# Performance work log

Hardware: AMD Instinct MI355X
Metric: run time of the kernel (lower is better)

Reference implementation:

```python
import jax, jax.numpy as jnp
import numpy as np

OBS = 128; N_AGENT = 16; N_ACTION = 8; N_LAYER = 2; HID = 128
GE = 256; LE = 256; F1 = 512; F2 = 512


def _edges(batch_size, n):
    # all ordered pairs (i, j), i != j, within each sample; GCNConv adds self-loops
    i, j = np.meshgrid(np.arange(n), np.arange(n), indexing='ij')
    m = i != j
    src0, dst0 = i[m], j[m]                      # [n*(n-1)]
    off = (np.arange(batch_size) * n)[:, None]
    src = (src0[None, :] + off).reshape(-1)
    dst = (dst0[None, :] + off).reshape(-1)
    return jnp.asarray(src, jnp.int32), jnp.asarray(dst, jnp.int32)


def setup_inputs() -> dict:
    key = jax.random.key(0)
    ks = jax.random.split(key, 16)
    g = lambda k, shp, fan: jax.random.normal(k, shp, jnp.float32) / np.sqrt(fan)
    return {
        'obs_j': jax.random.normal(ks[0], (2048, N_AGENT, OBS), jnp.float32),
        'W_pre': g(ks[1], (OBS, HID), OBS), 'b_pre': jnp.zeros((HID,), jnp.float32),
        'W_gcn': g(ks[2], (N_LAYER, HID, HID), HID), 'b_gcn': jnp.zeros((N_LAYER, HID), jnp.float32),
        'W_post': g(ks[3], (HID, GE), HID), 'b_post': jnp.zeros((GE,), jnp.float32),
        'W_loc': g(ks[4], (OBS, LE), OBS), 'b_loc': jnp.zeros((LE,), jnp.float32),
        'W1': g(ks[5], (GE + LE, F1), GE + LE), 'b1': jnp.zeros((F1,), jnp.float32),
        'W2': g(ks[6], (F1, F2), F1), 'b2': jnp.zeros((F2,), jnp.float32),
        'W3': g(ks[7], (F2, N_ACTION), F2), 'b3': jnp.zeros((N_ACTION,), jnp.float32),
    }


def reference(obs_j, W_pre, b_pre, W_gcn, b_gcn, W_post, b_post,
              W_loc, b_loc, W1, b1, W2, b2, W3, b3):
    B, n, _ = obs_j.shape
    N = B * n
    obs = obs_j.reshape(N, OBS)
    x = jax.nn.relu(obs @ W_pre + b_pre)          # [N, HID]

    src, dst = _edges(B, n)
    # GCNConv with self-loops on a fully-connected graph: deg = n for every node,
    # edge norm = 1/sqrt(deg_i*deg_j) = 1/n for every (A+I) edge.
    inv_n = jnp.float32(1.0) / n
    for l in range(N_LAYER):
        h = x @ W_gcn[l]                          # lin (no bias inside propagate)
        agg = jax.ops.segment_sum(h[src], dst, num_segments=N)  # neighbor gather/scatter
        x = jax.nn.relu((agg + h) * inv_n + b_gcn[l])            # + self-loop msg, bias

    g = x.reshape(B, n, HID).mean(axis=1)         # global_mean_pool over each graph
    g = jax.nn.relu(g @ W_post + b_post)          # [B, GE]
    loc = jax.nn.relu(obs @ W_loc + b_loc)        # [B*n, LE]
    gi = jnp.repeat(g, n, axis=0)                 # repeat_interleave over agents
    z = jnp.concatenate([gi, loc], axis=1)
    z = jax.nn.relu(z @ W1 + b1)
    z = jax.nn.relu(z @ W2 + b2)
    q = z @ W3 + b3
    return q.reshape(B, n, N_ACTION)
```

## Files before the change

kernel.cpp:

```cpp
#include <hip/hip_runtime.h>
#include <hip/hip_bf16.h>
#include <stdint.h>

typedef __bf16 bf16;
typedef __bf16 bf16x4 __attribute__((ext_vector_type(4)));
typedef __bf16 bf16x8 __attribute__((ext_vector_type(8)));
typedef float f32x4 __attribute__((ext_vector_type(4)));

#define BM 128
#define BN 128
#define BK 64

#define GL(p) ((const __attribute__((address_space(1))) void*)(p))
#define SH(p) ((__attribute__((address_space(3))) void*)(p))

__device__ inline void tp(const float* W, bf16* WT, int id, int shiftK, int N) {
  int K = 1 << shiftK;
  int n = id >> shiftK;
  int k = id & (K - 1);
  WT[id] = (bf16)W[(size_t)k * N + n];
}

__global__ __launch_bounds__(256) void prep_all(
    const float* __restrict__ W1, const float* __restrict__ W2,
    bf16* __restrict__ W1T, bf16* __restrict__ W2T,
    const float* __restrict__ Wpre, const float* __restrict__ Wloc,
    const float* __restrict__ Wgcn, const float* __restrict__ Wpost,
    bf16* __restrict__ WpreLocT, bf16* __restrict__ Wg0T, bf16* __restrict__ Wg1T,
    bf16* __restrict__ WpostT,
    const float* __restrict__ bpre, const float* __restrict__ bloc,
    float* __restrict__ biasPL, float* __restrict__ outq) {
  __shared__ bf16 tile[64 * 68];
  int blk = blockIdx.x;
  int tid = threadIdx.x;
  if (blk < 128) {
    const float* W = (blk < 64) ? W1 : W2;
    bf16* WT = (blk < 64) ? W1T : W2T;
    int t = blk & 63;
    int tk0 = (t >> 3) * 64, tn0 = (t & 7) * 64;
#pragma unroll
    for (int p = 0; p < 4; p++) {
      int kr = p * 16 + (tid >> 4), nc = (tid & 15) * 4;
      float4 f = *(const float4*)(W + (size_t)(tk0 + kr) * 512 + tn0 + nc);
      bf16x4 v; v[0] = (bf16)f.x; v[1] = (bf16)f.y; v[2] = (bf16)f.z; v[3] = (bf16)f.w;
      *(bf16x4*)&tile[kr * 68 + nc] = v;
    }
    __syncthreads();
#pragma unroll
    for (int p = 0; p < 4; p++) {
      int nr = p * 16 + (tid >> 4), kc = (tid & 15) * 4;
      bf16x4 v;
#pragma unroll
      for (int i = 0; i < 4; i++) v[i] = tile[(kc + i) * 68 + nr];
      *(bf16x4*)(WT + (size_t)(tn0 + nr) * 512 + tk0 + kc) = v;
    }
    return;
  }
  blk -= 128;
  if (blk < 448) {
    int id = blk * 256 + tid;
    if (id < 16384) { tp(Wpre, WpreLocT, id, 7, 128); return; } id -= 16384;
    if (id < 32768) { tp(Wloc, WpreLocT + 16384, id, 7, 256); return; } id -= 32768;
    if (id < 16384) { tp(Wgcn, Wg0T, id, 7, 128); return; } id -= 16384;
    if (id < 16384) { tp(Wgcn + 16384, Wg1T, id, 7, 128); return; } id -= 16384;
    tp(Wpost, WpostT, id, 7, 256);
    return;
  }
  blk -= 448;
  if (blk == 0) {
    if (tid < 128) biasPL[tid] = bpre[tid];
    biasPL[128 + tid] = bloc[tid];
    return;
  }
  blk -= 1;
  float4 z = {0.f, 0.f, 0.f, 0.f};
#pragma unroll
  for (int i = 0; i < 4; i++)
    ((float4*)outq)[(size_t)blk * 1024 + i * 256 + tid] = z;
}

template <int NT, int ASRC, bool POOL, bool QFUSE>
__global__ __launch_bounds__(256, 4) void gemm_k(
    const float* __restrict__ Af, const bf16* __restrict__ Ab, const bf16* __restrict__ Ag,
    const bf16* __restrict__ BT, const float* __restrict__ bias,
    bf16* __restrict__ C, int ldc, bf16* __restrict__ pool_out,
    const float* __restrict__ W3, const float* __restrict__ b3, float* __restrict__ outq,
    int M, int K) {
  __shared__ bf16 smem[16384];
  bf16* As = smem;
  bf16* Bs = smem + 8192;

  const int tid = threadIdx.x;
  const int id = blockIdx.x;
  const int s = id >> 3;
  const int n_idx = s % NT;
  const int m0 = ((id & 7) + 8 * (s / NT)) * BM;
  const int n0 = n_idx * BN;

  f32x4 acc[4][4] = {};

  const int lane = tid & 63;
  const int wave = tid >> 6;
  const int wm = (wave >> 1) * 64;
  const int wn = (wave & 1) * 64;
  const int lm = lane & 15;
  const int quad = lane >> 4;

  for (int k0 = 0; k0 < K; k0 += BK) {
#pragma unroll
    for (int it = 0; it < 4; it++) {
      int idx = it * 256 + tid;
      int row = idx >> 3;
      int c = idx & 7;
      int cv8 = c ^ (row & 7);
      int kk = k0 + cv8 * 8;
      if (ASRC == 1) {
        const float* src = Af + (size_t)(m0 + row) * K + kk;
        float4 f0 = *(const float4*)src;
        float4 f1 = *(const float4*)(src + 4);
        bf16x8 v;
        v[0] = (bf16)f0.x; v[1] = (bf16)f0.y; v[2] = (bf16)f0.z; v[3] = (bf16)f0.w;
        v[4] = (bf16)f1.x; v[5] = (bf16)f1.y; v[6] = (bf16)f1.z; v[7] = (bf16)f1.w;
        *(bf16x8*)&As[row * 64 + c * 8] = v;
      } else {
        const bf16* ga;
        if (ASRC == 2) {
          int r = m0 + row;
          ga = (k0 < 256) ? (Ag + (size_t)(r >> 4) * 256 + kk)
                          : (Ab + (size_t)r * 256 + (kk - 256));
        } else {
          ga = Ab + (size_t)(m0 + row) * K + kk;
        }
        __builtin_amdgcn_global_load_lds(GL(ga), SH(&As[(idx & ~63) * 8]), 16, 0, 0);
      }
      const bf16* gb = BT + (size_t)(n0 + row) * K + kk;
      __builtin_amdgcn_global_load_lds(GL(gb), SH(&Bs[(idx & ~63) * 8]), 16, 0, 0);
    }
    __syncthreads();

#pragma unroll
    for (int ks = 0; ks < 2; ks++) {
      const int ua = quad + ks * 4;
      bf16x8 a[4], b[4];
#pragma unroll
      for (int i = 0; i < 4; i++) {
        int r = wm + lm + i * 16;
        a[i] = *(const bf16x8*)&As[r * 64 + ((ua ^ (r & 7)) * 8)];
      }
#pragma unroll
      for (int j = 0; j < 4; j++) {
        int r = wn + lm + j * 16;
        b[j] = *(const bf16x8*)&Bs[r * 64 + ((ua ^ (r & 7)) * 8)];
      }
#pragma unroll
      for (int i = 0; i < 4; i++)
#pragma unroll
        for (int j = 0; j < 4; j++)
          acc[i][j] = __builtin_amdgcn_mfma_f32_16x16x32_bf16(a[i], b[j], acc[i][j], 0, 0, 0);
    }
    __syncthreads();
  }

  if (POOL && n_idx == 0) {
#pragma unroll
    for (int i = 0; i < 4; i++) {
      int sample = (m0 + wm + i * 16) >> 4;
#pragma unroll
      for (int j = 0; j < 4; j++) {
        int col = wn + j * 16 + lm;
        float b = bias[col];
        float v = 0.f;
#pragma unroll
        for (int r = 0; r < 4; r++) v += fmaxf(acc[i][j][r] + b, 0.f);
        v += __shfl_xor(v, 16);
        v += __shfl_xor(v, 32);
        if (quad == 0) pool_out[(size_t)sample * 128 + col] = (bf16)(v * 0.0625f);
      }
    }
  } else if (QFUSE) {
#pragma unroll
    for (int i = 0; i < 4; i++)
#pragma unroll
      for (int j = 0; j < 4; j++) {
        int col = wn + j * 16 + lm;
        float b = bias[n0 + col];
#pragma unroll
        for (int r = 0; r < 4; r++) {
          int row = wm + i * 16 + quad * 4 + r;
          smem[row * 128 + col] = (bf16)fmaxf(acc[i][j][r] + b, 0.f);
        }
      }
    __syncthreads();
    int n = lane & 7;
    int kg = lane >> 3;
    float w3r[16];
#pragma unroll
    for (int i = 0; i < 16; i++) w3r[i] = W3[(size_t)(n0 + kg * 16 + i) * 8 + n];
    float bn = (n_idx == 0) ? b3[n] : 0.f;
    int rbase = wave * 32;
    for (int rr = 0; rr < 32; rr++) {
      const bf16* zr = &smem[(rbase + rr) * 128 + kg * 16];
      bf16x8 z0 = *(const bf16x8*)zr;
      bf16x8 z1v = *(const bf16x8*)(zr + 8);
      float v = 0.f;
#pragma unroll
      for (int i = 0; i < 8; i++) v += (float)z0[i] * w3r[i];
#pragma unroll
      for (int i = 0; i < 8; i++) v += (float)z1v[i] * w3r[8 + i];
      v += __shfl_down(v, 32);
      v += __shfl_down(v, 16);
      v += __shfl_down(v, 8);
      if (lane < 8) atomicAdd(&outq[(size_t)(m0 + rbase + rr) * 8 + n], v + bn);
    }
  } else {
#pragma unroll
    for (int i = 0; i < 4; i++)
#pragma unroll
      for (int j = 0; j < 4; j++) {
        int col = wn + j * 16 + lm;
        float b = bias[n0 + col];
#pragma unroll
        for (int r = 0; r < 4; r++) {
          int row = wm + i * 16 + quad * 4 + r;
          smem[row * 128 + col] = (bf16)fmaxf(acc[i][j][r] + b, 0.f);
        }
      }
    __syncthreads();
    const int coff = POOL ? (n0 - 128) : n0;
#pragma unroll
    for (int c = 0; c < 8; c++) {
      int ci = c * 256 + tid;
      int row = ci >> 4, col8 = (ci & 15) * 8;
      *(bf16x8*)&C[(size_t)(m0 + row) * ldc + coff + col8] = *(const bf16x8*)&smem[row * 128 + col8];
    }
  }
}

__global__ __launch_bounds__(256) void gcn_chain(
    const bf16* __restrict__ xbar, const bf16* __restrict__ Wg0T,
    const bf16* __restrict__ Wg1T, const bf16* __restrict__ WpostT,
    const float* __restrict__ b_gcn, const float* __restrict__ b_post,
    bf16* __restrict__ g) {
  __shared__ bf16 xs[16 * 136];
  __shared__ bf16 ws[256 * 136];
  const int tid = threadIdx.x;
  const int lane = tid & 63, wave = tid >> 6;
  const int lm = lane & 15, quad = lane >> 4;
  const int rb = blockIdx.x * 16;

  {
    int row = tid >> 4, cv = (tid & 15) * 8;
    *(bf16x8*)&xs[row * 136 + cv] = *(const bf16x8*)&xbar[(size_t)(rb + row) * 128 + cv];
  }

  const bf16* Wl[3] = {Wg0T, Wg1T, WpostT};
  const float* bl[3] = {b_gcn, b_gcn + 128, b_post};
  const int Nl[3] = {128, 128, 256};

  for (int l = 0; l < 3; l++) {
    const int N = Nl[l];
    __syncthreads();
    for (int c = tid; c < N * 16; c += 256) {
      int row = c >> 4, cv = (c & 15) * 8;
      *(bf16x8*)&ws[row * 136 + cv] = *(const bf16x8*)&Wl[l][(size_t)row * 128 + cv];
    }
    __syncthreads();
    const int nj = N / 64;
    f32x4 acc[4] = {};
#pragma unroll
    for (int kk = 0; kk < 128; kk += 32) {
      bf16x8 a = *(const bf16x8*)&xs[lm * 136 + quad * 8 + kk];
      for (int j = 0; j < nj; j++) {
        int col = (wave * nj + j) * 16 + lm;
        bf16x8 b = *(const bf16x8*)&ws[col * 136 + quad * 8 + kk];
        acc[j] = __builtin_amdgcn_mfma_f32_16x16x32_bf16(a, b, acc[j], 0, 0, 0);
      }
    }
    __syncthreads();
    const float* bias = bl[l];
    if (l < 2) {
      for (int j = 0; j < nj; j++) {
        int col = (wave * nj + j) * 16 + lm;
        float bv = bias[col];
#pragma unroll
        for (int r = 0; r < 4; r++)
          xs[(quad * 4 + r) * 136 + col] = (bf16)fmaxf(acc[j][r] + bv, 0.f);
      }
    } else {
      for (int j = 0; j < nj; j++) {
        int col = (wave * nj + j) * 16 + lm;
        float bv = bias[col];
#pragma unroll
        for (int r = 0; r < 4; r++)
          g[(size_t)(rb + quad * 4 + r) * 256 + col] = (bf16)fmaxf(acc[j][r] + bv, 0.f);
      }
    }
  }
}

extern "C" void kernel_launch(void* const* d_in, const int* in_sizes, int n_in,
                              void* d_out, int out_size, void* d_ws, size_t ws_size,
                              hipStream_t stream) {
  const float* obs    = (const float*)d_in[0];
  const float* W_pre  = (const float*)d_in[1];
  const float* b_pre  = (const float*)d_in[2];
  const float* W_gcn  = (const float*)d_in[3];
  const float* b_gcn  = (const float*)d_in[4];
  const float* W_post = (const float*)d_in[5];
  const float* b_post = (const float*)d_in[6];
  const float* W_loc  = (const float*)d_in[7];
  const float* b_loc  = (const float*)d_in[8];
  const float* W1     = (const float*)d_in[9];
  const float* b1     = (const float*)d_in[10];
  const float* W2     = (const float*)d_in[11];
  const float* b2     = (const float*)d_in[12];
  const float* W3     = (const float*)d_in[13];
  const float* b3     = (const float*)d_in[14];
  float* out = (float*)d_out;

  char* p = (char*)d_ws;
  auto alloc = [&](size_t bytes) { char* r = p; p += (bytes + 255) & ~(size_t)255; return r; };
  bf16* WpreLocT = (bf16*)alloc(384 * 128 * 2);
  float* biasPL  = (float*)alloc(384 * 4);
  bf16* Wg0T   = (bf16*)alloc(128 * 128 * 2);
  bf16* Wg1T   = (bf16*)alloc(128 * 128 * 2);
  bf16* WpostT = (bf16*)alloc(256 * 128 * 2);
  bf16* W1T    = (bf16*)alloc(512 * 512 * 2);
  bf16* W2T    = (bf16*)alloc(512 * 512 * 2);
  bf16* xbar   = (bf16*)alloc(2048 * 128 * 2);
  bf16* loc    = (bf16*)alloc((size_t)32768 * 256 * 2);
  bf16* g      = (bf16*)alloc(2048 * 256 * 2);
  bf16* z1     = (bf16*)alloc((size_t)32768 * 512 * 2);

  prep_all<<<641, 256, 0, stream>>>(W1, W2, W1T, W2T,
                                    W_pre, W_loc, W_gcn, W_post,
                                    WpreLocT, Wg0T, Wg1T, WpostT,
                                    b_pre, b_loc, biasPL, out);
  gemm_k<3, 1, true, false><<<768, 256, 0, stream>>>(
      obs, nullptr, nullptr, WpreLocT, biasPL, loc, 256, xbar,
      nullptr, nullptr, nullptr, 32768, 128);
  gcn_chain<<<128, 256, 0, stream>>>(xbar, Wg0T, Wg1T, WpostT, b_gcn, b_post, g);
  gemm_k<4, 2, false, false><<<1024, 256, 0, stream>>>(
      nullptr, loc, g, W1T, b1, z1, 512, nullptr,
      nullptr, nullptr, nullptr, 32768, 512);
  gemm_k<4, 0, false, true><<<1024, 256, 0, stream>>>(
      nullptr, z1, nullptr, W2T, b2, nullptr, 0, nullptr,
      W3, b3, out, 32768, 512);
}
```

Measured before the change: 174.3 us.

## Fuse GCN chain into first GEMM's pooling blocks, removing a kernel launch

The separate gcn_chain kernel is removed. The n_idx==0 blocks of the first GEMM now take their pooled 8-sample tile (padded to 16 rows) and run the two GCN layers and the post-projection with MFMA in the same block, writing g directly. The xbar round trip and one launch go away, and the GEMM kernels are specialised with compile-time K. In exchange, a third of the first kernel's blocks do extra serial work with weights read straight from global memory, and half of each MFMA tile is wasted on padding rows.

Result: faster. 169.3 us (-2.9%).

```diff
diff --git a/kernel.cpp b/kernel.cpp
--- a/kernel.cpp
+++ b/kernel.cpp
@@ -7,10 +7,7 @@
 typedef __bf16 bf16x8 __attribute__((ext_vector_type(8)));
 typedef float f32x4 __attribute__((ext_vector_type(4)));
 
-#define BM 128
-#define BN 128
-#define BK 64
-
+#define MFMA(a, b, c) __builtin_amdgcn_mfma_f32_16x16x32_bf16(a, b, c, 0, 0, 0)
 #define GL(p) ((const __attribute__((address_space(1))) void*)(p))
 #define SH(p) ((__attribute__((address_space(3))) void*)(p))
 
@@ -79,13 +76,13 @@
     ((float4*)outq)[(size_t)blk * 1024 + i * 256 + tid] = z;
 }
 
-template <int NT, int ASRC, bool POOL, bool QFUSE>
-__global__ __launch_bounds__(256, 4) void gemm_k(
-    const float* __restrict__ Af, const bf16* __restrict__ Ab, const bf16* __restrict__ Ag,
-    const bf16* __restrict__ BT, const float* __restrict__ bias,
-    bf16* __restrict__ C, int ldc, bf16* __restrict__ pool_out,
-    const float* __restrict__ W3, const float* __restrict__ b3, float* __restrict__ outq,
-    int M, int K) {
+__global__ __launch_bounds__(256, 4) void k1c(
+    const float* __restrict__ obs, const bf16* __restrict__ WpreLocT,
+    const float* __restrict__ biasPL,
+    const bf16* __restrict__ Wg0T, const bf16* __restrict__ Wg1T,
+    const bf16* __restrict__ WpostT, const float* __restrict__ b_gcn,
+    const float* __restrict__ b_post,
+    bf16* __restrict__ loc, bf16* __restrict__ g) {
   __shared__ bf16 smem[16384];
   bf16* As = smem;
   bf16* Bs = smem + 8192;
@@ -93,20 +90,16 @@
   const int tid = threadIdx.x;
   const int id = blockIdx.x;
   const int s = id >> 3;
-  const int n_idx = s % NT;
-  const int m0 = ((id & 7) + 8 * (s / NT)) * BM;
-  const int n0 = n_idx * BN;
+  const int n_idx = s % 3;
+  const int m0 = ((id & 7) + 8 * (s / 3)) * 128;
+  const int n0 = n_idx * 128;
 
   f32x4 acc[4][4] = {};
-
-  const int lane = tid & 63;
-  const int wave = tid >> 6;
-  const int wm = (wave >> 1) * 64;
-  const int wn = (wave & 1) * 64;
-  const int lm = lane & 15;
-  const int quad = lane >> 4;
-
-  for (int k0 = 0; k0 < K; k0 += BK) {
+  const int lane = tid & 63, wave = tid >> 6;
+  const int wm = (wave >> 1) * 64, wn = (wave & 1) * 64;
+  const int lm = lane & 15, quad = lane >> 4;
+
+  for (int k0 = 0; k0 < 128; k0 += 64) {
 #pragma unroll
     for (int it = 0; it < 4; it++) {
       int idx = it * 256 + tid;
@@ -114,30 +107,17 @@
       int c = idx & 7;
       int cv8 = c ^ (row & 7);
       int kk = k0 + cv8 * 8;
-      if (ASRC == 1) {
-        const float* src = Af + (size_t)(m0 + row) * K + kk;
-        float4 f0 = *(const float4*)src;
-        float4 f1 = *(const float4*)(src + 4);
-        bf16x8 v;
-        v[0] = (bf16)f0.x; v[1] = (bf16)f0.y; v[2] = (bf16)f0.z; v[3] = (bf16)f0.w;
-        v[4] = (bf16)f1.x; v[5] = (bf16)f1.y; v[6] = (bf16)f1.z; v[7] = (bf16)f1.w;
-        *(bf16x8*)&As[row * 64 + c * 8] = v;
-      } else {
-        const bf16* ga;
-        if (ASRC == 2) {
-          int r = m0 + row;
-          ga = (k0 < 256) ? (Ag + (size_t)(r >> 4) * 256 + kk)
-                          : (Ab + (size_t)r * 256 + (kk - 256));
-        } else {
-          ga = Ab + (size_t)(m0 + row) * K + kk;
-        }
-        __builtin_amdgcn_global_load_lds(GL(ga), SH(&As[(idx & ~63) * 8]), 16, 0, 0);
-      }
-      const bf16* gb = BT + (size_t)(n0 + row) * K + kk;
+      const float* src = obs + (size_t)(m0 + row) * 128 + kk;
+      float4 f0 = *(const float4*)src;
+      float4 f1 = *(const float4*)(src + 4);
+      bf16x8 v;
+      v[0] = (bf16)f0.x; v[1] = (bf16)f0.y; v[2] = (bf16)f0.z; v[3] = (bf16)f0.w;
+      v[4] = (bf16)f1.x; v[5] = (bf16)f1.y; v[6] = (bf16)f1.z; v[7] = (bf16)f1.w;
+      *(bf16x8*)&As[row * 64 + c * 8] = v;
+      const bf16* gb = WpreLocT + (size_t)(n0 + row) * 128 + kk;
       __builtin_amdgcn_global_load_lds(GL(gb), SH(&Bs[(idx & ~63) * 8]), 16, 0, 0);
     }
     __syncthreads();
-
 #pragma unroll
     for (int ks = 0; ks < 2; ks++) {
       const int ua = quad + ks * 4;
@@ -156,38 +136,204 @@
       for (int i = 0; i < 4; i++)
 #pragma unroll
         for (int j = 0; j < 4; j++)
-          acc[i][j] = __builtin_amdgcn_mfma_f32_16x16x32_bf16(a[i], b[j], acc[i][j], 0, 0, 0);
-    }
-    __syncthreads();
-  }
-
-  if (POOL && n_idx == 0) {
+          acc[i][j] = MFMA(a[i], b[j], acc[i][j]);
+    }
+    __syncthreads();
+  }
+
+  if (n_idx == 0) {
+    bf16* xs = smem;
+    bf16* x2 = smem + 2176;
 #pragma unroll
     for (int i = 0; i < 4; i++) {
-      int sample = (m0 + wm + i * 16) >> 4;
+      int sl = (wave >> 1) * 4 + i;
 #pragma unroll
       for (int j = 0; j < 4; j++) {
         int col = wn + j * 16 + lm;
-        float b = bias[col];
+        float bb = biasPL[col];
         float v = 0.f;
 #pragma unroll
-        for (int r = 0; r < 4; r++) v += fmaxf(acc[i][j][r] + b, 0.f);
+        for (int r = 0; r < 4; r++) v += fmaxf(acc[i][j][r] + bb, 0.f);
         v += __shfl_xor(v, 16);
         v += __shfl_xor(v, 32);
-        if (quad == 0) pool_out[(size_t)sample * 128 + col] = (bf16)(v * 0.0625f);
-      }
-    }
-  } else if (QFUSE) {
+        if (quad == 0) xs[sl * 136 + col] = (bf16)(v * 0.0625f);
+        else if (quad == 1) xs[(8 + sl) * 136 + col] = (bf16)0.f;
+      }
+    }
+    __syncthreads();
+    {
+      f32x4 c2[2] = {};
+#pragma unroll
+      for (int ku = 0; ku < 4; ++ku) {
+        bf16x8 a = *(const bf16x8*)&xs[lm * 136 + (ku * 4 + quad) * 8];
+#pragma unroll
+        for (int jn = 0; jn < 2; ++jn) {
+          int col = (wave * 2 + jn) * 16 + lm;
+          bf16x8 b = *(const bf16x8*)&Wg0T[(size_t)col * 128 + ku * 32 + quad * 8];
+          c2[jn] = MFMA(a, b, c2[jn]);
+        }
+      }
+      __syncthreads();
+#pragma unroll
+      for (int jn = 0; jn < 2; ++jn) {
+        int col = (wave * 2 + jn) * 16 + lm;
+        float bb = b_gcn[col];
+#pragma unroll
+        for (int r = 0; r < 4; ++r)
+          x2[(quad * 4 + r) * 136 + col] = (bf16)fmaxf(c2[jn][r] + bb, 0.f);
+      }
+    }
+    __syncthreads();
+    {
+      f32x4 c2[2] = {};
+#pragma unroll
+      for (int ku = 0; ku < 4; ++ku) {
+        bf16x8 a = *(const bf16x8*)&x2[lm * 136 + (ku * 4 + quad) * 8];
+#pragma unroll
+        for (int jn = 0; jn < 2; ++jn) {
+          int col = (wave * 2 + jn) * 16 + lm;
+          bf16x8 b = *(const bf16x8*)&Wg1T[(size_t)col * 128 + ku * 32 + quad * 8];
+          c2[jn] = MFMA(a, b, c2[jn]);
+        }
+      }
+      __syncthreads();
+#pragma unroll
+      for (int jn = 0; jn < 2; ++jn) {
+        int col = (wave * 2 + jn) * 16 + lm;
+        float bb = b_gcn[128 + col];
+#pragma unroll
+        for (int r = 0; r < 4; ++r)
+          xs[(quad * 4 + r) * 136 + col] = (bf16)fmaxf(c2[jn][r] + bb, 0.f);
+      }
+    }
+    __syncthreads();
+    {
+      f32x4 c3[4] = {};
+#pragma unroll
+      for (int ku = 0; ku < 4; ++ku) {
+        bf16x8 a = *(const bf16x8*)&xs[lm * 136 + (ku * 4 + quad) * 8];
+#pragma unroll
+        for (int jn = 0; jn < 4; ++jn) {
+          int col = (wave * 4 + jn) * 16 + lm;
+          bf16x8 b = *(const bf16x8*)&WpostT[(size_t)col * 128 + ku * 32 + quad * 8];
+          c3[jn] = MFMA(a, b, c3[jn]);
+        }
+      }
+      int sample0 = m0 >> 4;
+#pragma unroll
+      for (int jn = 0; jn < 4; ++jn) {
+        int col = (wave * 4 + jn) * 16 + lm;
+        float bb = b_post[col];
+#pragma unroll
+        for (int r = 0; r < 4; ++r) {
+          int row = quad * 4 + r;
+          if (row < 8)
+            g[(size_t)(sample0 + row) * 256 + col] = (bf16)fmaxf(c3[jn][r] + bb, 0.f);
+        }
+      }
+    }
+  } else {
 #pragma unroll
     for (int i = 0; i < 4; i++)
 #pragma unroll
       for (int j = 0; j < 4; j++) {
         int col = wn + j * 16 + lm;
-        float b = bias[n0 + col];
+        float bb = biasPL[n0 + col];
 #pragma unroll
         for (int r = 0; r < 4; r++) {
           int row = wm + i * 16 + quad * 4 + r;
-          smem[row * 128 + col] = (bf16)fmaxf(acc[i][j][r] + b, 0.f);
+          smem[row * 128 + col] = (bf16)fmaxf(acc[i][j][r] + bb, 0.f);
+        }
+      }
+    __syncthreads();
+    const int coff = n0 - 128;
+#pragma unroll
+    for (int c = 0; c < 8; c++) {
+      int ci = c * 256 + tid;
+      int row = ci >> 4, col8 = (ci & 15) * 8;
+      *(bf16x8*)&loc[(size_t)(m0 + row) * 256 + coff + col8] = *(const bf16x8*)&smem[row * 128 + col8];
+    }
+  }
+}
+
+template <int ASRC, bool QFUSE>
+__global__ __launch_bounds__(256, 4) void gemm_k(
+    const bf16* __restrict__ Ab, const bf16* __restrict__ Ag,
+    const bf16* __restrict__ BT, const float* __restrict__ bias,
+    bf16* __restrict__ C,
+    const float* __restrict__ W3, const float* __restrict__ b3,
+    float* __restrict__ outq) {
+  __shared__ bf16 smem[16384];
+  bf16* As = smem;
+  bf16* Bs = smem + 8192;
+
+  const int tid = threadIdx.x;
+  const int id = blockIdx.x;
+  const int s = id >> 3;
+  const int n_idx = s & 3;
+  const int m0 = ((id & 7) + 8 * (s >> 2)) * 128;
+  const int n0 = n_idx * 128;
+
+  f32x4 acc[4][4] = {};
+  const int lane = tid & 63, wave = tid >> 6;
+  const int wm = (wave >> 1) * 64, wn = (wave & 1) * 64;
+  const int lm = lane & 15, quad = lane >> 4;
+
+  for (int k0 = 0; k0 < 512; k0 += 64) {
+#pragma unroll
+    for (int it = 0; it < 4; it++) {
+      int idx = it * 256 + tid;
+      int row = idx >> 3;
+      int c = idx & 7;
+      int cv8 = c ^ (row & 7);
+      int kk = k0 + cv8 * 8;
+      const bf16* ga;
+      if (ASRC == 2) {
+        int r = m0 + row;
+        ga = (k0 < 256) ? (Ag + (size_t)(r >> 4) * 256 + kk)
+                        : (Ab + (size_t)r * 256 + (kk - 256));
+      } else {
+        ga = Ab + (size_t)(m0 + row) * 512 + kk;
+      }
+      __builtin_amdgcn_global_load_lds(GL(ga), SH(&As[(idx & ~63) * 8]), 16, 0, 0);
+      const bf16* gb = BT + (size_t)(n0 + row) * 512 + kk;
+      __builtin_amdgcn_global_load_lds(GL(gb), SH(&Bs[(idx & ~63) * 8]), 16, 0, 0);
+    }
+    __syncthreads();
+#pragma unroll
+    for (int ks = 0; ks < 2; ks++) {
+      const int ua = quad + ks * 4;
+      bf16x8 a[4], b[4];
+#pragma unroll
+      for (int i = 0; i < 4; i++) {
+        int r = wm + lm + i * 16;
+        a[i] = *(const bf16x8*)&As[r * 64 + ((ua ^ (r & 7)) * 8)];
+      }
+#pragma unroll
+      for (int j = 0; j < 4; j++) {
+        int r = wn + lm + j * 16;
+        b[j] = *(const bf16x8*)&Bs[r * 64 + ((ua ^ (r & 7)) * 8)];
+      }
+#pragma unroll
+      for (int i = 0; i < 4; i++)
+#pragma unroll
+        for (int j = 0; j < 4; j++)
+          acc[i][j] = MFMA(a[i], b[j], acc[i][j]);
+    }
+    __syncthreads();
+  }
+
+  if (QFUSE) {
+#pragma unroll
+    for (int i = 0; i < 4; i++)
+#pragma unroll
+      for (int j = 0; j < 4; j++) {
+        int col = wn + j * 16 + lm;
+        float bb = bias[n0 + col];
+#pragma unroll
+        for (int r = 0; r < 4; r++) {
+          int row = wm + i * 16 + quad * 4 + r;
+          smem[row * 128 + col] = (bf16)fmaxf(acc[i][j][r] + bb, 0.f);
         }
       }
     __syncthreads();
@@ -218,82 +364,19 @@
 #pragma unroll
       for (int j = 0; j < 4; j++) {
         int col = wn + j * 16 + lm;
-        float b = bias[n0 + col];
+        float bb = bias[n0 + col];
 #pragma unroll
         for (int r = 0; r < 4; r++) {
           int row = wm + i * 16 + quad * 4 + r;
-          smem[row * 128 + col] = (bf16)fmaxf(acc[i][j][r] + b, 0.f);
-        }
-      }
-    __syncthreads();
-    const int coff = POOL ? (n0 - 128) : n0;
+          smem[row * 128 + col] = (bf16)fmaxf(acc[i][j][r] + bb, 0.f);
+        }
+      }
+    __syncthreads();
 #pragma unroll
     for (int c = 0; c < 8; c++) {
       int ci = c * 256 + tid;
       int row = ci >> 4, col8 = (ci & 15) * 8;
-      *(bf16x8*)&C[(size_t)(m0 + row) * ldc + coff + col8] = *(const bf16x8*)&smem[row * 128 + col8];
-    }
-  }
-}
-
-__global__ __launch_bounds__(256) void gcn_chain(
-    const bf16* __restrict__ xbar, const bf16* __restrict__ Wg0T,
-    const bf16* __restrict__ Wg1T, const bf16* __restrict__ WpostT,
-    const float* __restrict__ b_gcn, const float* __restrict__ b_post,
-    bf16* __restrict__ g) {
-  __shared__ bf16 xs[16 * 136];
-  __shared__ bf16 ws[256 * 136];
-  const int tid = threadIdx.x;
-  const int lane = tid & 63, wave = tid >> 6;
-  const int lm = lane & 15, quad = lane >> 4;
-  const int rb = blockIdx.x * 16;
-
-  {
-    int row = tid >> 4, cv = (tid & 15) * 8;
-    *(bf16x8*)&xs[row * 136 + cv] = *(const bf16x8*)&xbar[(size_t)(rb + row) * 128 + cv];
-  }
-
-  const bf16* Wl[3] = {Wg0T, Wg1T, WpostT};
-  const float* bl[3] = {b_gcn, b_gcn + 128, b_post};
-  const int Nl[3] = {128, 128, 256};
-
-  for (int l = 0; l < 3; l++) {
-    const int N = Nl[l];
-    __syncthreads();
-    for (int c = tid; c < N * 16; c += 256) {
-      int row = c >> 4, cv = (c & 15) * 8;
-      *(bf16x8*)&ws[row * 136 + cv] = *(const bf16x8*)&Wl[l][(size_t)row * 128 + cv];
-    }
-    __syncthreads();
-    const int nj = N / 64;
-    f32x4 acc[4] = {};
-#pragma unroll
-    for (int kk = 0; kk < 128; kk += 32) {
-      bf16x8 a = *(const bf16x8*)&xs[lm * 136 + quad * 8 + kk];
-      for (int j = 0; j < nj; j++) {
-        int col = (wave * nj + j) * 16 + lm;
-        bf16x8 b = *(const bf16x8*)&ws[col * 136 + quad * 8 + kk];
-        acc[j] = __builtin_amdgcn_mfma_f32_16x16x32_bf16(a, b, acc[j], 0, 0, 0);
-      }
-    }
-    __syncthreads();
-    const float* bias = bl[l];
-    if (l < 2) {
-      for (int j = 0; j < nj; j++) {
-        int col = (wave * nj + j) * 16 + lm;
-        float bv = bias[col];
-#pragma unroll
-        for (int r = 0; r < 4; r++)
-          xs[(quad * 4 + r) * 136 + col] = (bf16)fmaxf(acc[j][r] + bv, 0.f);
-      }
-    } else {
-      for (int j = 0; j < nj; j++) {
-        int col = (wave * nj + j) * 16 + lm;
-        float bv = bias[col];
-#pragma unroll
-        for (int r = 0; r < 4; r++)
-          g[(size_t)(rb + quad * 4 + r) * 256 + col] = (bf16)fmaxf(acc[j][r] + bv, 0.f);
-      }
+      *(bf16x8*)&C[(size_t)(m0 + row) * 512 + n0 + col8] = *(const bf16x8*)&smem[row * 128 + col8];
     }
   }
 }
@@ -327,23 +410,19 @@
   bf16* WpostT = (bf16*)alloc(256 * 128 * 2);
   bf16* W1T    = (bf16*)alloc(512 * 512 * 2);
   bf16* W2T    = (bf16*)alloc(512 * 512 * 2);
-  bf16* xbar   = (bf16*)alloc(2048 * 128 * 2);
-  bf16* loc    = (bf16*)alloc((size_t)32768 * 256 * 2);
-  bf16* g      = (bf16*)alloc(2048 * 256 * 2);
-  bf16* z1     = (bf16*)alloc((size_t)32768 * 512 * 2);
+  bf16* locB   = (bf16*)alloc((size_t)32768 * 256 * 2);
+  bf16* gB     = (bf16*)alloc(2048 * 256 * 2);
+  bf16* z1B    = (bf16*)alloc((size_t)32768 * 512 * 2);
 
   prep_all<<<641, 256, 0, stream>>>(W1, W2, W1T, W2T,
                                     W_pre, W_loc, W_gcn, W_post,
                                     WpreLocT, Wg0T, Wg1T, WpostT,
                                     b_pre, b_loc, biasPL, out);
-  gemm_k<3, 1, true, false><<<768, 256, 0, stream>>>(
-      obs, nullptr, nullptr, WpreLocT, biasPL, loc, 256, xbar,
-      nullptr, nullptr, nullptr, 32768, 128);
-  gcn_chain<<<128, 256, 0, stream>>>(xbar, Wg0T, Wg1T, WpostT, b_gcn, b_post, g);
-  gemm_k<4, 2, false, false><<<1024, 256, 0, stream>>>(
-      nullptr, loc, g, W1T, b1, z1, 512, nullptr,
-      nullptr, nullptr, nullptr, 32768, 512);
-  gemm_k<4, 0, false, true><<<1024, 256, 0, stream>>>(
-      nullptr, z1, nullptr, W2T, b2, nullptr, 0, nullptr,
-      W3, b3, out, 32768, 512);
+  k1c<<<768, 256, 0, stream>>>(obs, WpreLocT, biasPL,
+                               Wg0T, Wg1T, WpostT, b_gcn, b_post,
+                               locB, gB);
+  gemm_k<2, false><<<1024, 256, 0, stream>>>(locB, gB, W1T, b1, z1B,
+                                             nullptr, nullptr, nullptr);
+  gemm_k<0, true><<<1024, 256, 0, stream>>>(z1B, nullptr, W2T, b2, nullptr,
+                                            W3, b3, out);
 }
```
